# Performance work log

Measured on AMD Instinct MI355X. Metric: run time of the kernel, lower is better.

The kernel has to match this reference:

```python
import jax, jax.numpy as jnp
import numpy as np

B, IN, OUT, ORDER = 8192, 1024, 1024, 7


def setup_inputs() -> dict:
    key = jax.random.key(0)
    k1, k2 = jax.random.split(key)
    x = jax.random.normal(k1, (B, IN), dtype=jnp.float32)
    tanh_range = jnp.float32(1.0)
    coef = jax.random.normal(k2, (OUT, IN, ORDER + 1), dtype=jnp.float32) * 0.1
    return {"x": x, "tanh_range": tanh_range, "coef": coef}


def _poly(x, tanh_range, order):
    # t^0, t^1, ..., t^order via cumulative products (matches torch recurrence)
    t = jnp.tanh(x * tanh_range)                      # [B, IN]
    powers = jnp.cumprod(jnp.broadcast_to(t[..., None], t.shape + (order,)), axis=-1)
    ones = jnp.ones_like(t)[..., None]
    return jnp.concatenate([ones, powers], axis=-1)   # [B, IN, order+1]


def reference(x, tanh_range, coef):
    poly = _poly(x, tanh_range, ORDER)                # [B, IN, K]
    # output[b, j] = sum_{i,k} coef[j,i,k] * poly[b,i,k]
    return jnp.einsum('bik,jik->bj', poly, coef)
```

## Files before the change

kernel.cpp:

```cpp
#include <hip/hip_runtime.h>
#include <hip/hip_bf16.h>


#define KT 7168
#define KFULL 8192

#define BM 128
#define BN 128
#define BK 128

typedef short bf16x8 __attribute__((ext_vector_type(8)));
typedef short bf16x4 __attribute__((ext_vector_type(4)));
typedef float f32x4  __attribute__((ext_vector_type(4)));

__device__ __forceinline__ unsigned short f2bf(float f) {
    union { __hip_bfloat16 h; unsigned short u; } v;
    v.h = __float2bfloat16(f);
    return v.u;
}

__device__ __forceinline__ void gload_lds16(const void* gp, void* lp) {
    __builtin_amdgcn_global_load_lds(
        (const __attribute__((address_space(1))) void*)gp,
        (__attribute__((address_space(3))) void*)lp, 16, 0, 0);
}

#define CVT_BLOCKS  512
#define TANH_BLOCKS 4096

__global__ __launch_bounds__(256)
void prep(const float* __restrict__ x, const float* __restrict__ trp,
          const float* __restrict__ coef, unsigned short* __restrict__ coef_bf,
          unsigned short* __restrict__ A, float* __restrict__ bias) {
    __shared__ float redbuf[4];

    const int t   = threadIdx.x;
    const int blk = blockIdx.x;
    const int rl  = t >> 7;
    const int ig  = t & 127;

    if (blk < CVT_BLOCKS) {
        const int j = blk * 2 + rl;
        const float* src = coef + (size_t)j * KFULL + ig * 64;
        float k0sum = 0.f;
        bf16x8 pl[7];
        #pragma unroll
        for (int i = 0; i < 8; ++i) {
            const float4 f0 = *(const float4*)(src + i * 8);
            const float4 f1 = *(const float4*)(src + i * 8 + 4);
            k0sum += f0.x;
            pl[0][i] = (short)f2bf(f0.y); pl[1][i] = (short)f2bf(f0.z);
            pl[2][i] = (short)f2bf(f0.w); pl[3][i] = (short)f2bf(f1.x);
            pl[4][i] = (short)f2bf(f1.y); pl[5][i] = (short)f2bf(f1.z);
            pl[6][i] = (short)f2bf(f1.w);
        }
        #pragma unroll
        for (int off = 32; off > 0; off >>= 1) k0sum += __shfl_down(k0sum, off, 64);
        if ((t & 63) == 0) redbuf[t >> 6] = k0sum;
        __syncthreads();
        if (t == 0)   bias[j] = redbuf[0] + redbuf[1];
        if (t == 128) bias[j] = redbuf[2] + redbuf[3];

        unsigned short* dst = coef_bf + (size_t)j * KT + ig * 8;
        #pragma unroll
        for (int p = 0; p < 7; ++p)
            *(bf16x8*)(dst + p * 1024) = pl[p];
    } else {
        const int bb = (blk - CVT_BLOCKS) * 2 + rl;
        const float tr = trp[0];
        const float* xp = x + (size_t)bb * 1024 + ig * 8;
        const float4 x0 = *(const float4*)xp;
        const float4 x1 = *(const float4*)(xp + 4);
        const float xs[8] = {x0.x, x0.y, x0.z, x0.w, x1.x, x1.y, x1.z, x1.w};
        bf16x8 pl[7];
        #pragma unroll
        for (int i = 0; i < 8; ++i) {
            const float e  = __expf(2.0f * tr * xs[i]);
            const float tt = 1.0f - 2.0f * __builtin_amdgcn_rcpf(e + 1.0f);
            float pw = tt;
            #pragma unroll
            for (int p = 0; p < 7; ++p) { pl[p][i] = (short)f2bf(pw); pw *= tt; }
        }
        unsigned short* dst = A + (size_t)bb * KT + ig * 8;
        #pragma unroll
        for (int p = 0; p < 7; ++p)
            *(bf16x8*)(dst + p * 1024) = pl[p];
    }
}

__global__ __launch_bounds__(256, 2)
void gemm_bt(const unsigned short* __restrict__ A, const unsigned short* __restrict__ Bt,
             const float* __restrict__ bias, float* __restrict__ out)
{
    __shared__ unsigned short As[BM * BK];
    __shared__ unsigned short Bs[BN * BK];

    const int t    = threadIdx.x;
    const int m0   = blockIdx.x * BM;
    const int n0   = blockIdx.y * BN;
    const int w    = t >> 6;
    const int lane = t & 63;
    const int wm   = (w >> 1) * 64;
    const int wn   = (w & 1) * 64;
    const int lrow = lane & 15;

    const int bid = blockIdx.x + (int)blockIdx.y * 64;
    if (bid & 256) __builtin_amdgcn_s_sleep(19);

    const int srow   = t >> 4;
    const int schunk = (t & 15) ^ srow;
    const int wbase  = w * 512;

    f32x4 acc[4][4];
    #pragma unroll
    for (int i = 0; i < 4; i++)
        #pragma unroll
        for (int j = 0; j < 4; j++)
            acc[i][j] = (f32x4){0.f, 0.f, 0.f, 0.f};

    const size_t abase = (size_t)(m0 + srow) * KT + schunk * 8;
    const size_t bbase = (size_t)(n0 + srow) * KT + schunk * 8;

    for (int k0 = 0; k0 < KT; k0 += BK) {
        #pragma unroll
        for (int r = 0; r < 8; ++r)
            gload_lds16(A + abase + (size_t)r * 16 * KT + k0, &As[r * 2048 + wbase]);
        #pragma unroll
        for (int r = 0; r < 8; ++r)
            gload_lds16(Bt + bbase + (size_t)r * 16 * KT + k0, &Bs[r * 2048 + wbase]);

        __syncthreads();

        #pragma unroll
        for (int kk = 0; kk < BK; kk += 32) {
            const int soff = ((((kk >> 3) + (lane >> 4)) ^ (lane & 15)) * 8);
            bf16x8 a[4], b[4];
            #pragma unroll
            for (int i = 0; i < 4; i++)
                a[i] = *(const bf16x8*)&As[(wm + i * 16 + lrow) * BK + soff];
            #pragma unroll
            for (int j = 0; j < 4; j++)
                b[j] = *(const bf16x8*)&Bs[(wn + j * 16 + lrow) * BK + soff];
            #pragma unroll
            for (int i = 0; i < 4; i++)
                #pragma unroll
                for (int j = 0; j < 4; j++)
                    acc[i][j] = __builtin_amdgcn_mfma_f32_16x16x32_bf16(a[i], b[j], acc[i][j], 0, 0, 0);
        }

        __syncthreads();
    }

    const int crow = (lane >> 4) * 4;
    const int ccol = lane & 15;
    #pragma unroll
    for (int j = 0; j < 4; j++) {
        const int n = n0 + wn + j * 16 + ccol;
        const float bv = bias[n];
        #pragma unroll
        for (int i = 0; i < 4; i++) {
            const int m = m0 + wm + i * 16 + crow;
            #pragma unroll
            for (int r = 0; r < 4; ++r)
                out[(size_t)(m + r) * 1024 + n] = acc[i][j][r] + bv;
        }
    }
}

#define LDK 72
__global__ __launch_bounds__(256, 2)
void taylor_gemm(const float* __restrict__ x, const float* __restrict__ trp,
                 const float* __restrict__ coef, float* __restrict__ out)
{
    __shared__ unsigned short Afs[BM * LDK];
    __shared__ unsigned short Bfs[BN * LDK];

    const int t  = threadIdx.x;
    const int m0 = blockIdx.x * BM;
    const int n0 = blockIdx.y * BN;
    const float tr = trp[0];

    const int w    = t >> 6;
    const int lane = t & 63;
    const int wm   = (w >> 1) * 64;
    const int wn   = (w & 1) * 64;
    const int lrow = lane & 15;
    const int kq   = (lane >> 4) * 8;

    f32x4 acc[4][4];
    #pragma unroll
    for (int i = 0; i < 4; i++)
        #pragma unroll
        for (int j = 0; j < 4; j++)
            acc[i][j] = (f32x4){0.f, 0.f, 0.f, 0.f};

    const int bcol  = t & 15;
    const int brow0 = t >> 4;
    const int acol  = t & 7;
    const int arow0 = t >> 3;

    for (int k0 = 0; k0 < KFULL; k0 += 64) {
        const int i0 = k0 >> 3;
        #pragma unroll
        for (int r = 0; r < 8; ++r) {
            const int row = brow0 + r * 16;
            const float4 v = *(const float4*)(coef + (size_t)(n0 + row) * KFULL + k0 + bcol * 4);
            bf16x4 pk;
            pk[0] = (short)f2bf(v.x); pk[1] = (short)f2bf(v.y);
            pk[2] = (short)f2bf(v.z); pk[3] = (short)f2bf(v.w);
            *(bf16x4*)&Bfs[row * LDK + bcol * 4] = pk;
        }
        #pragma unroll
        for (int r = 0; r < 4; ++r) {
            const int row = arow0 + r * 32;
            const float xv = x[(size_t)(m0 + row) * 1024 + i0 + acol];
            const float e  = __expf(2.0f * tr * xv);
            const float tt = 1.0f - 2.0f / (e + 1.0f);
            bf16x8 pk;
            float p = 1.0f;
            #pragma unroll
            for (int k = 0; k < 8; ++k) { pk[k] = (short)f2bf(p); p *= tt; }
            *(bf16x8*)&Afs[row * LDK + acol * 8] = pk;
        }
        __syncthreads();
        #pragma unroll
        for (int kk = 0; kk < 64; kk += 32) {
            bf16x8 a[4], b[4];
            #pragma unroll
            for (int i = 0; i < 4; i++)
                a[i] = *(const bf16x8*)&Afs[(wm + i * 16 + lrow) * LDK + kk + kq];
            #pragma unroll
            for (int j = 0; j < 4; j++)
                b[j] = *(const bf16x8*)&Bfs[(wn + j * 16 + lrow) * LDK + kk + kq];
            #pragma unroll
            for (int i = 0; i < 4; i++)
                #pragma unroll
                for (int j = 0; j < 4; j++)
                    acc[i][j] = __builtin_amdgcn_mfma_f32_16x16x32_bf16(a[i], b[j], acc[i][j], 0, 0, 0);
        }
        __syncthreads();
    }

    const int crow = (lane >> 4) * 4;
    const int ccol = lane & 15;
    #pragma unroll
    for (int i = 0; i < 4; i++) {
        #pragma unroll
        for (int j = 0; j < 4; j++) {
            const int m = m0 + wm + i * 16 + crow;
            const int n = n0 + wn + j * 16 + ccol;
            #pragma unroll
            for (int r = 0; r < 4; ++r)
                out[(size_t)(m + r) * 1024 + n] = acc[i][j][r];
        }
    }
}

extern "C" void kernel_launch(void* const* d_in, const int* in_sizes, int n_in,
                              void* d_out, int out_size, void* d_ws, size_t ws_size,
                              hipStream_t stream) {
    const float* x    = (const float*)d_in[0];
    const float* trp  = (const float*)d_in[1];
    const float* coef = (const float*)d_in[2];
    float* out = (float*)d_out;

    const size_t A_BYTES    = (size_t)8192 * KT * 2;
    const size_t COEF_BYTES = (size_t)1024 * KT * 2;
    const size_t BIAS_BYTES = 1024 * sizeof(float);

    if (ws_size >= A_BYTES + COEF_BYTES + BIAS_BYTES) {
        unsigned short* A_bf    = (unsigned short*)d_ws;
        unsigned short* coef_bf = (unsigned short*)((char*)d_ws + A_BYTES);
        float*          bias    = (float*)((char*)d_ws + A_BYTES + COEF_BYTES);

        prep<<<dim3(CVT_BLOCKS + TANH_BLOCKS), dim3(256), 0, stream>>>(
            x, trp, coef, coef_bf, A_bf, bias);
        gemm_bt<<<dim3(8192 / BM, 1024 / BN), dim3(256), 0, stream>>>(
            A_bf, coef_bf, bias, out);
    } else {
        taylor_gemm<<<dim3(8192 / BM, 1024 / BN), dim3(256), 0, stream>>>(x, trp, coef, out);
    }
}
```

Before: 230.2 us.

## Split K across warps in gemm_bt with LDS partial-sum reduction

```diff
diff --git a/kernel.cpp b/kernel.cpp
--- a/kernel.cpp
+++ b/kernel.cpp
@@ -92,28 +92,27 @@
 void gemm_bt(const unsigned short* __restrict__ A, const unsigned short* __restrict__ Bt,
              const float* __restrict__ bias, float* __restrict__ out)
 {
-    __shared__ unsigned short As[BM * BK];
-    __shared__ unsigned short Bs[BN * BK];
+    __shared__ unsigned short lds[BM * BK + BN * BK];
+    unsigned short* As = lds;
+    unsigned short* Bs = lds + BM * BK;
 
     const int t    = threadIdx.x;
     const int m0   = blockIdx.x * BM;
     const int n0   = blockIdx.y * BN;
     const int w    = t >> 6;
     const int lane = t & 63;
-    const int wm   = (w >> 1) * 64;
-    const int wn   = (w & 1) * 64;
+    const int nh   = w & 1;
+    const int ks   = w >> 1;
+    const int wn   = nh * 64;
     const int lrow = lane & 15;
-
-    const int bid = blockIdx.x + (int)blockIdx.y * 64;
-    if (bid & 256) __builtin_amdgcn_s_sleep(19);
 
     const int srow   = t >> 4;
     const int schunk = (t & 15) ^ srow;
     const int wbase  = w * 512;
 
-    f32x4 acc[4][4];
+    f32x4 acc[8][4];
     #pragma unroll
-    for (int i = 0; i < 4; i++)
+    for (int i = 0; i < 8; i++)
         #pragma unroll
         for (int j = 0; j < 4; j++)
             acc[i][j] = (f32x4){0.f, 0.f, 0.f, 0.f};
@@ -132,17 +131,18 @@
         __syncthreads();
 
         #pragma unroll
-        for (int kk = 0; kk < BK; kk += 32) {
+        for (int kh = 0; kh < 2; ++kh) {
+            const int kk = ks * 64 + kh * 32;
             const int soff = ((((kk >> 3) + (lane >> 4)) ^ (lane & 15)) * 8);
-            bf16x8 a[4], b[4];
-            #pragma unroll
-            for (int i = 0; i < 4; i++)
-                a[i] = *(const bf16x8*)&As[(wm + i * 16 + lrow) * BK + soff];
+            bf16x8 a[8], b[4];
+            #pragma unroll
+            for (int i = 0; i < 8; i++)
+                a[i] = *(const bf16x8*)&As[(i * 16 + lrow) * BK + soff];
             #pragma unroll
             for (int j = 0; j < 4; j++)
                 b[j] = *(const bf16x8*)&Bs[(wn + j * 16 + lrow) * BK + soff];
             #pragma unroll
-            for (int i = 0; i < 4; i++)
+            for (int i = 0; i < 8; i++)
                 #pragma unroll
                 for (int j = 0; j < 4; j++)
                     acc[i][j] = __builtin_amdgcn_mfma_f32_16x16x32_bf16(a[i], b[j], acc[i][j], 0, 0, 0);
@@ -153,16 +153,38 @@
 
     const int crow = (lane >> 4) * 4;
     const int ccol = lane & 15;
-    #pragma unroll
-    for (int j = 0; j < 4; j++) {
-        const int n = n0 + wn + j * 16 + ccol;
-        const float bv = bias[n];
-        #pragma unroll
-        for (int i = 0; i < 4; i++) {
-            const int m = m0 + wm + i * 16 + crow;
-            #pragma unroll
-            for (int r = 0; r < 4; ++r)
-                out[(size_t)(m + r) * 1024 + n] = acc[i][j][r] + bv;
+    float* pbuf = (float*)lds;
+
+    if (ks == 1) {
+        float* pb = pbuf + nh * 8192;
+        #pragma unroll
+        for (int j = 0; j < 4; j++) {
+            const int nl = j * 16 + ccol;
+            const int xr = (nl & 7) << 2;
+            #pragma unroll
+            for (int i = 0; i < 8; i++) {
+                const int mb = (i * 16 + crow) ^ xr;
+                *(f32x4*)&pb[nl * 128 + mb] = acc[i][j];
+            }
+        }
+    }
+    __syncthreads();
+    if (ks == 0) {
+        const float* pb = pbuf + nh * 8192;
+        #pragma unroll
+        for (int j = 0; j < 4; j++) {
+            const int nl = j * 16 + ccol;
+            const int n  = n0 + wn + nl;
+            const float bv = bias[n];
+            const int xr = (nl & 7) << 2;
+            #pragma unroll
+            for (int i = 0; i < 8; i++) {
+                const int mb = i * 16 + crow;
+                const f32x4 p = *(const f32x4*)&pb[nl * 128 + (mb ^ xr)];
+                #pragma unroll
+                for (int r = 0; r < 4; ++r)
+                    out[(size_t)(m0 + mb + r) * 1024 + n] = acc[i][j][r] + p[r] + bv;
+            }
         }
     }
 }
```

Result: no change. 230.9 us (+0.3%).
